# Performance work log

Measured on AMD Instinct MI355X. Metric: run time of the kernel, lower is better.

The kernel has to match this reference:

```python
import jax, jax.numpy as jnp
import numpy as np

P = 16           # patch size
E = P * P        # embed dim of MHA (must equal dim)
NH = 4           # num heads
HD = E // NH     # head dim


def setup_inputs() -> dict:
    key = jax.random.key(0)
    k1, k2, k3, k4, k5 = jax.random.split(key, 5)
    B, C, H, W = 2, 256, 256, 256
    scale = 1.0 / np.sqrt(E)
    return {
        "x": jax.random.normal(k1, (B, C, H, W), dtype=jnp.float32),
        "w_in": jax.random.normal(k2, (3 * E, E), dtype=jnp.float32) * scale,
        "b_in": jnp.zeros((3 * E,), dtype=jnp.float32),
        "w_out": jax.random.normal(k3, (E, E), dtype=jnp.float32) * scale,
        "b_out": jnp.zeros((E,), dtype=jnp.float32),
    }


def reference(x, w_in, b_in, w_out, b_out):
    B, C, H, W = x.shape
    nP = (H // P) * (W // P)
    # x.unfold(2,p,p).unfold(3,p,p).reshape(B,C,-1,p*p)
    patches = (
        x.reshape(B, C, H // P, P, W // P, P)
        .transpose(0, 1, 2, 4, 3, 5)
        .reshape(B, C, nP, E)
    )
    # permute(0,2,1,3).reshape(B*nP, C, p*p): batch=B*nP, seq=C, embed=E
    t = patches.transpose(0, 2, 1, 3).reshape(B * nP, C, E)

    qkv = t @ w_in.T + b_in                      # (N, C, 3E)
    q, k, v = jnp.split(qkv, 3, axis=-1)

    def to_heads(a):  # (N, C, E) -> (N, NH, C, HD)
        return a.reshape(B * nP, C, NH, HD).transpose(0, 2, 1, 3)

    q, k, v = to_heads(q), to_heads(k), to_heads(v)
    scores = jnp.einsum("nhqd,nhkd->nhqk", q * (HD ** -0.5), k)
    attn = jax.nn.softmax(scores, axis=-1)
    o = jnp.einsum("nhqk,nhkd->nhqd", attn, v)   # (N, NH, C, HD)
    o = o.transpose(0, 2, 1, 3).reshape(B * nP, C, E)
    o = o @ w_out.T + b_out
    # reshape(B, -1, C, p*p).permute(0, 2, 1, 3)
    return o.reshape(B, nP, C, E).transpose(0, 2, 1, 3)
```

## Files before the change

kernel.cpp:

```cpp
#include <hip/hip_runtime.h>
#include <hip/hip_bf16.h>

typedef __attribute__((ext_vector_type(8))) short s16x8;
typedef __attribute__((ext_vector_type(4))) float f32x4;

#define WS_SEG 67108864ULL

#if defined(__has_attribute)
#if __has_attribute(amdgpu_num_vgpr)
#define VGPR_CAP_128 __attribute__((amdgpu_num_vgpr(128)))
#else
#define VGPR_CAP_128
#endif
#else
#define VGPR_CAP_128
#endif

static __device__ __forceinline__ unsigned short f2bf(float f) {
    return __builtin_bit_cast(unsigned short, __float2bfloat16(f));
}
static __device__ __forceinline__ unsigned int pack2(float a, float b) {
    return (unsigned int)f2bf(a) | ((unsigned int)f2bf(b) << 16);
}
static __device__ __forceinline__ s16x8 u4cast(uint4 u) {
    return __builtin_bit_cast(s16x8, u);
}
static __device__ __forceinline__ void gl_lds16(const void* g, void* l) {
    __builtin_amdgcn_global_load_lds(
        (const __attribute__((address_space(1))) unsigned int*)g,
        (__attribute__((address_space(3))) unsigned int*)l, 16, 0, 0);
}

__global__ __launch_bounds__(256) void convw_frag(const float* __restrict__ wi,
                                                  unsigned short* __restrict__ wp) {
    int o8 = blockIdx.x * 256 + threadIdx.x;
    int nkc = o8 >> 10;
    int rem = o8 & 1023;
    int row = rem >> 2;
    int lk8 = (rem & 3) * 8;
    int Ni = nkc >> 3, kk = (nkc >> 1) & 3, kc = nkc & 1;
    const float* src = wi + ((size_t)(Ni * 256 + row)) * 256 + kk * 64 + kc * 32 + lk8;
    float4 a = *reinterpret_cast<const float4*>(src);
    float4 b = *reinterpret_cast<const float4*>(src + 4);
    uint4 o = { pack2(a.x, a.y), pack2(a.z, a.w), pack2(b.x, b.y), pack2(b.z, b.w) };
    *reinterpret_cast<uint4*>(wp + o8 * 8) = o;
}

__global__ __launch_bounds__(256) void convw_swz(const float* __restrict__ wi,
                                                 unsigned short* __restrict__ wb) {
    int i = (blockIdx.x * 256 + threadIdx.x) * 4;
    float4 v = *reinterpret_cast<const float4*>(wi + i);
    int bb = i * 2;
    int row = i >> 8;
    int dst = (bb & ~127) | ((bb & 127) ^ ((row & 7) << 4));
    uint2 o = { pack2(v.x, v.y), pack2(v.z, v.w) };
    *reinterpret_cast<uint2*>((char*)wb + dst) = o;
}

__global__ __launch_bounds__(256) void gather_swz(const float* __restrict__ x,
                                                  unsigned short* __restrict__ t) {
    int q = (blockIdx.x * 256 + threadIdx.x) * 4;
    int e = q & 255, c = (q >> 8) & 255, n = q >> 16;
    int b = n >> 8, p = n & 255;
    int xi = ((b * 256 + c) * 256 + (p >> 4) * 16 + (e >> 4)) * 256 + (p & 15) * 16 + (e & 15);
    float4 v = *reinterpret_cast<const float4*>(x + xi);
    int bb = q * 2;
    int row = q >> 8;
    int dst = (bb & ~127) | ((bb & 127) ^ ((row & 7) << 4));
    uint2 o = { pack2(v.x, v.y), pack2(v.z, v.w) };
    *reinterpret_cast<uint2*>((char*)t + dst) = o;
}

__global__ __launch_bounds__(256) void qkv11(
    const unsigned short* __restrict__ Ab,
    const unsigned short* __restrict__ Wp,
    const float* __restrict__ bias,
    unsigned short* __restrict__ Qo, unsigned short* __restrict__ Ko,
    unsigned short* __restrict__ Vt)
{
    __shared__ __align__(16) char AsB[65536];

    const int t = threadIdx.x, w = t >> 6, lane = t & 63;
    const int lr = lane & 15, lk = lane >> 4;
    const int wm = w >> 1, wn = w & 1;

    const int bm = blockIdx.x;
    const int n = bm >> 1;

    const char* Ag = (const char*)Ab + (size_t)bm * 65536;

    #pragma unroll
    for (int i = 0; i < 16; ++i) {
        int u = i * 256 + t;
        gl_lds16(Ag + u * 16, AsB + (i * 256 + w * 64) * 16);
    }
    __syncthreads();

    #pragma unroll 1
    for (int bn = 0; bn < 4; ++bn) {
        const int X = bn >> 1;
        const int half = bn & 1;
        f32x4 acc[4][4] = {};
        #pragma unroll
        for (int kk = 0; kk < 4; ++kk) {
            #pragma unroll
            for (int kc = 0; kc < 2; ++kc) {
                const char* wb = (const char*)Wp + (((X * 4 + kk) * 2 + kc) << 14);
                s16x8 bfr[4];
                #pragma unroll
                for (int fn = 0; fn < 4; ++fn)
                    bfr[fn] = *reinterpret_cast<const s16x8*>(
                        wb + ((half * 128 + wn * 64 + fn * 16 + lr) * 32 + lk * 8) * 2);
                s16x8 af[4];
                #pragma unroll
                for (int fm = 0; fm < 4; ++fm) {
                    int m = wm * 64 + fm * 16 + lr;
                    af[fm] = *reinterpret_cast<const s16x8*>(
                        AsB + m * 512 + kk * 128 + ((kc * 64 + lk * 16) ^ ((m & 7) << 4)));
                }
                __builtin_amdgcn_s_setprio(1);
                #pragma unroll
                for (int fm = 0; fm < 4; ++fm)
                    #pragma unroll
                    for (int fn = 0; fn < 4; ++fn)
                        acc[fm][fn] = __builtin_amdgcn_mfma_f32_16x16x32_bf16(bfr[fn], af[fm], acc[fm][fn], 0, 0, 0);
                __builtin_amdgcn_s_setprio(0);
            }
        }
        unsigned short* base = X ? Ko : Qo;
        const float qs = X ? 1.0f : 0.18033688011112042f;
        #pragma unroll
        for (int fn = 0; fn < 4; ++fn) {
            int col_local = wn * 64 + fn * 16 + lk * 4;
            int mc = half * 128 + col_local;
            f32x4 bv4 = *reinterpret_cast<const f32x4*>(bias + X * 256 + mc);
            int h = mc >> 6, d0 = mc & 63;
            #pragma unroll
            for (int fm = 0; fm < 4; ++fm) {
                int c = (bm & 1) * 128 + wm * 64 + fm * 16 + lr;
                uint2 st = { pack2((acc[fm][fn][0] + bv4[0]) * qs, (acc[fm][fn][1] + bv4[1]) * qs),
                             pack2((acc[fm][fn][2] + bv4[2]) * qs, (acc[fm][fn][3] + bv4[3]) * qs) };
                *reinterpret_cast<uint2*>(
                    (char*)base + (size_t)((n * 4 + h) * 256 + c) * 128 + d0 * 2) = st;
            }
        }
    }

    #pragma unroll 1
    for (int half = 0; half < 2; ++half) {
        f32x4 acc[4][4] = {};
        #pragma unroll
        for (int kk = 0; kk < 4; ++kk) {
            #pragma unroll
            for (int kc = 0; kc < 2; ++kc) {
                const char* wb = (const char*)Wp + (((2 * 4 + kk) * 2 + kc) << 14);
                s16x8 bfr[4];
                #pragma unroll
                for (int fn = 0; fn < 4; ++fn)
                    bfr[fn] = *reinterpret_cast<const s16x8*>(
                        wb + ((half * 128 + wn * 64 + fn * 16 + lr) * 32 + lk * 8) * 2);
                s16x8 af[4];
                #pragma unroll
                for (int fm = 0; fm < 4; ++fm) {
                    int m = wm * 64 + fm * 16 + lr;
                    af[fm] = *reinterpret_cast<const s16x8*>(
                        AsB + m * 512 + kk * 128 + ((kc * 64 + lk * 16) ^ ((m & 7) << 4)));
                }
                __builtin_amdgcn_s_setprio(1);
                #pragma unroll
                for (int fm = 0; fm < 4; ++fm)
                    #pragma unroll
                    for (int fn = 0; fn < 4; ++fn)
                        acc[fm][fn] = __builtin_amdgcn_mfma_f32_16x16x32_bf16(af[fm], bfr[fn], acc[fm][fn], 0, 0, 0);
                __builtin_amdgcn_s_setprio(0);
            }
        }
        #pragma unroll
        for (int fn = 0; fn < 4; ++fn) {
            int dcol_local = wn * 64 + fn * 16 + lr;
            int mc = half * 128 + dcol_local;
            float bv = bias[512 + mc];
            int h = mc >> 6, d = mc & 63;
            #pragma unroll
            for (int fm = 0; fm < 4; ++fm) {
                int c = (bm & 1) * 128 + wm * 64 + fm * 16 + lk * 4;
                uint2 st = { pack2(acc[fm][fn][0] + bv, acc[fm][fn][1] + bv),
                             pack2(acc[fm][fn][2] + bv, acc[fm][fn][3] + bv) };
                *reinterpret_cast<uint2*>(
                    (char*)Vt + (size_t)((n * 4 + h) * 64 + d) * 512 + c * 2) = st;
            }
        }
    }
}

__global__ __launch_bounds__(256) void gemm_out(
    const unsigned short* __restrict__ Ab,
    const unsigned short* __restrict__ Wb,
    const float* __restrict__ bias,
    float* __restrict__ Out)
{
    __shared__ __align__(16) char smem[32768];
    char* AsB = smem;
    char* BsB = smem + 16384;

    const int t = threadIdx.x, w = t >> 6, lane = t & 63;
    const int lr = lane & 15, lk = lane >> 4;
    const int wm = w >> 1, wn = w & 1;

    const int flat = blockIdx.x;
    const int xcd = flat & 7, idx = flat >> 3;
    const int bm = xcd * 128 + idx / 2;
    const int bn = idx % 2;

    const char* Ag = (const char*)Ab + (size_t)bm * 65536;
    const char* Bg = (const char*)Wb + (size_t)bn * 65536;

    f32x4 acc[4][4] = {};

    for (int kk = 0; kk < 4; ++kk) {
        #pragma unroll
        for (int i = 0; i < 4; ++i) {
            int u = (i * 4 + w) * 64 + lane;
            int row = u >> 3, cb = (u & 7) * 16;
            gl_lds16(Ag + row * 512 + kk * 128 + cb, AsB + (i * 4 + w) * 1024);
            gl_lds16(Bg + row * 512 + kk * 128 + cb, BsB + (i * 4 + w) * 1024);
        }
        __syncthreads();
        #pragma unroll
        for (int kc = 0; kc < 2; ++kc) {
            s16x8 af[4], bf[4];
            #pragma unroll
            for (int fm = 0; fm < 4; ++fm) {
                int r = wm * 64 + fm * 16 + lr;
                af[fm] = *reinterpret_cast<const s16x8*>(
                    AsB + r * 128 + ((kc * 64 + lk * 16) ^ ((r & 7) << 4)));
            }
            #pragma unroll
            for (int fn = 0; fn < 4; ++fn) {
                int cc = wn * 64 + fn * 16 + lr;
                bf[fn] = *reinterpret_cast<const s16x8*>(
                    BsB + cc * 128 + ((kc * 64 + lk * 16) ^ ((cc & 7) << 4)));
            }
            #pragma unroll
            for (int fm = 0; fm < 4; ++fm)
                #pragma unroll
                for (int fn = 0; fn < 4; ++fn)
                    acc[fm][fn] = __builtin_amdgcn_mfma_f32_16x16x32_bf16(bf[fn], af[fm], acc[fm][fn], 0, 0, 0);
        }
        if (kk < 3) __syncthreads();
    }

    #pragma unroll
    for (int fn = 0; fn < 4; ++fn) {
        int colg = bn * 128 + wn * 64 + fn * 16 + lk * 4;
        f32x4 bv4 = *reinterpret_cast<const f32x4*>(bias + colg);
        #pragma unroll
        for (int fm = 0; fm < 4; ++fm) {
            int rg = bm * 128 + wm * 64 + fm * 16 + lr;
            int nn = rg >> 8, c = rg & 255;
            int b = nn >> 8, p = nn & 255;
            f32x4 st = acc[fm][fn] + bv4;
            *reinterpret_cast<f32x4*>(
                Out + (((size_t)(b * 256 + c) * 256 + p) << 8) + colg) = st;
        }
    }
}

__global__ __launch_bounds__(1024) VGPR_CAP_128 void attn8(
    const unsigned short* __restrict__ Q,
    const unsigned short* __restrict__ K,
    const unsigned short* __restrict__ V,
    unsigned short* __restrict__ O)
{
    __shared__ __align__(16) char KsB[32768];
    __shared__ __align__(16) char VsB[32768];

    const int nh = blockIdx.x;
    const int n = nh >> 2, h = nh & 3;
    const int t = threadIdx.x, w = t >> 6, lane = t & 63;
    const int lr = lane & 15, lk = lane >> 4;

    const unsigned short* Qg = Q + (size_t)nh * 16384;
    const char* Kg = (const char*)K + (size_t)nh * 32768;
    const char* Vg = (const char*)V + (size_t)nh * 32768;

    #pragma unroll
    for (int i = 0; i < 2; ++i) {
        int u = i * 1024 + t;
        int row = u >> 3, cb = (u & 7) * 16;
        uint4 val = *reinterpret_cast<const uint4*>(Kg + u * 16);
        *reinterpret_cast<uint4*>(KsB + row * 128 + (cb ^ ((row & 7) << 4))) = val;
    }
    #pragma unroll
    for (int i = 0; i < 2; ++i) {
        int u = i * 1024 + t;
        int row = u >> 5, cb = (u & 31) * 16;
        uint4 val = *reinterpret_cast<const uint4*>(Vg + u * 16);
        *reinterpret_cast<uint4*>(VsB + row * 512 + (cb ^ ((row & 7) << 4))) = val;
    }
    __syncthreads();

    const int swz = (lr & 7) << 4;
    const int qt = w;

    s16x8 bq0 = *reinterpret_cast<const s16x8*>(Qg + (qt * 16 + lr) * 64 + lk * 8);
    s16x8 bq1 = *reinterpret_cast<const s16x8*>(Qg + (qt * 16 + lr) * 64 + 32 + lk * 8);

    f32x4 oacc[4] = {};
    float l = 0.f;

    #pragma unroll
    for (int kb = 0; kb < 8; ++kb) {
        const int rb0 = ((2 * kb) * 16 + lr) * 128;
        const int rb1 = ((2 * kb + 1) * 16 + lr) * 128;
        s16x8 a00 = *reinterpret_cast<const s16x8*>(KsB + rb0 + ((lk * 16) ^ swz));
        s16x8 a01 = *reinterpret_cast<const s16x8*>(KsB + rb0 + ((64 + lk * 16) ^ swz));
        s16x8 a10 = *reinterpret_cast<const s16x8*>(KsB + rb1 + ((lk * 16) ^ swz));
        s16x8 a11 = *reinterpret_cast<const s16x8*>(KsB + rb1 + ((64 + lk * 16) ^ swz));
        f32x4 s0 = { 0.f, 0.f, 0.f, 0.f }, s1 = { 0.f, 0.f, 0.f, 0.f };
        __builtin_amdgcn_s_setprio(1);
        s0 = __builtin_amdgcn_mfma_f32_16x16x32_bf16(a00, bq0, s0, 0, 0, 0);
        s0 = __builtin_amdgcn_mfma_f32_16x16x32_bf16(a01, bq1, s0, 0, 0, 0);
        s1 = __builtin_amdgcn_mfma_f32_16x16x32_bf16(a10, bq0, s1, 0, 0, 0);
        s1 = __builtin_amdgcn_mfma_f32_16x16x32_bf16(a11, bq1, s1, 0, 0, 0);
        __builtin_amdgcn_s_setprio(0);

        float p0 = exp2f(s0[0]), p1 = exp2f(s0[1]);
        float p2 = exp2f(s0[2]), p3 = exp2f(s0[3]);
        float p4 = exp2f(s1[0]), p5 = exp2f(s1[1]);
        float p6 = exp2f(s1[2]), p7 = exp2f(s1[3]);
        l += ((p0 + p1) + (p2 + p3)) + ((p4 + p5) + (p6 + p7));
        uint4 pk = { pack2(p0, p1), pack2(p2, p3), pack2(p4, p5), pack2(p6, p7) };
        s16x8 pf = u4cast(pk);

        __builtin_amdgcn_s_setprio(1);
        #pragma unroll
        for (int dt = 0; dt < 4; ++dt) {
            const char* vb = VsB + (dt * 16 + lr) * 512;
            uint2 v0 = *reinterpret_cast<const uint2*>(vb + ((kb * 64 + lk * 8) ^ swz));
            uint2 v1 = *reinterpret_cast<const uint2*>(vb + ((kb * 64 + lk * 8 + 32) ^ swz));
            uint4 uu = { v0.x, v0.y, v1.x, v1.y };
            oacc[dt] = __builtin_amdgcn_mfma_f32_16x16x32_bf16(u4cast(uu), pf, oacc[dt], 0, 0, 0);
        }
        __builtin_amdgcn_s_setprio(0);
    }

    l += __shfl_xor(l, 16);
    l += __shfl_xor(l, 32);
    const float rl = 1.0f / l;

    char* orow = (char*)O + (size_t)(n * 256 + qt * 16 + lr) * 512 + h * 128;
    #pragma unroll
    for (int dt = 0; dt < 4; ++dt) {
        uint2 st = { pack2(oacc[dt][0] * rl, oacc[dt][1] * rl),
                     pack2(oacc[dt][2] * rl, oacc[dt][3] * rl) };
        *reinterpret_cast<uint2*>(orow + ((dt * 32 + lk * 8) ^ swz)) = st;
    }
}

extern "C" void kernel_launch(void* const* d_in, const int* in_sizes, int n_in,
                              void* d_out, int out_size, void* d_ws, size_t ws_size,
                              hipStream_t stream) {
    const float* x     = (const float*)d_in[0];
    const float* w_in  = (const float*)d_in[1];
    const float* b_in  = (const float*)d_in[2];
    const float* w_out = (const float*)d_in[3];
    const float* b_out = (const float*)d_in[4];

    char* ws = (char*)d_ws;
    unsigned short* tO = (unsigned short*)(ws);
    unsigned short* Qw = (unsigned short*)(ws + WS_SEG);
    unsigned short* Kw = (unsigned short*)(ws + 2 * WS_SEG);
    unsigned short* Vw = (unsigned short*)(ws + 3 * WS_SEG);

    unsigned short* WbIn = (unsigned short*)((float*)d_out + out_size - 98304);

    convw_frag<<<96, 256, 0, stream>>>(w_in, WbIn);
    gather_swz<<<32768, 256, 0, stream>>>(x, tO);

    qkv11<<<1024, 256, 0, stream>>>(tO, WbIn, b_in, Qw, Kw, Vw);

    attn8<<<2048, 1024, 0, stream>>>(Qw, Kw, Vw, tO);

    unsigned short* WbOut = Kw;
    convw_swz<<<64, 256, 0, stream>>>(w_out, WbOut);

    gemm_out<<<2048, 256, 0, stream>>>(tO, WbOut, b_out, (float*)d_out);
}
```

Before: 321.7 us.

## Split QKV GEMM into per-N-tile blocks reading fragment-packed A directly from global

The gather kernel now writes the token matrix in MFMA fragment-packed order (per 128-row tile, per 32-wide k chunk), so the QKV kernel can load A fragments straight from global memory without staging through 64KB of LDS. The QKV GEMM is split from 1024 blocks that each loop over six output tiles into 6144 blocks that each compute one tile. Blocks are remapped so that the six blocks sharing an A tile land on the same XCD, to get L2 reuse. This cuts LDS use and raises occupancy and parallelism, at the cost of reading A six times from cache/global instead of once into LDS.

```diff
diff --git a/kernel.cpp b/kernel.cpp
--- a/kernel.cpp
+++ b/kernel.cpp
@@ -57,84 +57,82 @@
     *reinterpret_cast<uint2*>((char*)wb + dst) = o;
 }
 
-__global__ __launch_bounds__(256) void gather_swz(const float* __restrict__ x,
-                                                  unsigned short* __restrict__ t) {
+__global__ __launch_bounds__(256) void gather_frag(const float* __restrict__ x,
+                                                   unsigned short* __restrict__ tp) {
     int q = (blockIdx.x * 256 + threadIdx.x) * 4;
     int e = q & 255, c = (q >> 8) & 255, n = q >> 16;
     int b = n >> 8, p = n & 255;
     int xi = ((b * 256 + c) * 256 + (p >> 4) * 16 + (e >> 4)) * 256 + (p & 15) * 16 + (e & 15);
     float4 v = *reinterpret_cast<const float4*>(x + xi);
-    int bb = q * 2;
-    int row = q >> 8;
-    int dst = (bb & ~127) | ((bb & 127) ^ ((row & 7) << 4));
+    int mrow = n * 256 + c;
+    int mt = mrow >> 7, m = mrow & 127;
+    int kk = e >> 6, kc = (e >> 5) & 1, ke = e & 31;
+    size_t dst = ((size_t)(mt * 8 + kk * 2 + kc) << 13) + (size_t)(m * 32 + ke) * 2;
     uint2 o = { pack2(v.x, v.y), pack2(v.z, v.w) };
-    *reinterpret_cast<uint2*>((char*)t + dst) = o;
-}
-
-__global__ __launch_bounds__(256) void qkv11(
-    const unsigned short* __restrict__ Ab,
+    *reinterpret_cast<uint2*>((char*)tp + dst) = o;
+}
+
+__global__ __launch_bounds__(256) void qkv12(
+    const unsigned short* __restrict__ Tp,
     const unsigned short* __restrict__ Wp,
     const float* __restrict__ bias,
     unsigned short* __restrict__ Qo, unsigned short* __restrict__ Ko,
     unsigned short* __restrict__ Vt)
 {
-    __shared__ __align__(16) char AsB[65536];
-
     const int t = threadIdx.x, w = t >> 6, lane = t & 63;
     const int lr = lane & 15, lk = lane >> 4;
     const int wm = w >> 1, wn = w & 1;
 
-    const int bm = blockIdx.x;
-    const int n = bm >> 1;
-
-    const char* Ag = (const char*)Ab + (size_t)bm * 65536;
-
-    #pragma unroll
-    for (int i = 0; i < 16; ++i) {
-        int u = i * 256 + t;
-        gl_lds16(Ag + u * 16, AsB + (i * 256 + w * 64) * 16);
-    }
-    __syncthreads();
-
-    #pragma unroll 1
-    for (int bn = 0; bn < 4; ++bn) {
-        const int X = bn >> 1;
-        const int half = bn & 1;
-        f32x4 acc[4][4] = {};
-        #pragma unroll
-        for (int kk = 0; kk < 4; ++kk) {
-            #pragma unroll
-            for (int kc = 0; kc < 2; ++kc) {
-                const char* wb = (const char*)Wp + (((X * 4 + kk) * 2 + kc) << 14);
-                s16x8 bfr[4];
-                #pragma unroll
-                for (int fn = 0; fn < 4; ++fn)
-                    bfr[fn] = *reinterpret_cast<const s16x8*>(
-                        wb + ((half * 128 + wn * 64 + fn * 16 + lr) * 32 + lk * 8) * 2);
-                s16x8 af[4];
-                #pragma unroll
-                for (int fm = 0; fm < 4; ++fm) {
-                    int m = wm * 64 + fm * 16 + lr;
-                    af[fm] = *reinterpret_cast<const s16x8*>(
-                        AsB + m * 512 + kk * 128 + ((kc * 64 + lk * 16) ^ ((m & 7) << 4)));
-                }
-                __builtin_amdgcn_s_setprio(1);
+    const int flat = blockIdx.x;
+    const int xcd = flat & 7, idx = flat >> 3;
+    const int bm = xcd * 128 + idx / 6;
+    const int bn = idx % 6;
+    const int X = bn >> 1, half = bn & 1;
+
+    f32x4 acc[4][4] = {};
+
+    #pragma unroll
+    for (int kk = 0; kk < 4; ++kk) {
+        #pragma unroll
+        for (int kc = 0; kc < 2; ++kc) {
+            const char* tb = (const char*)Tp + ((size_t)(bm * 8 + kk * 2 + kc) << 13);
+            const char* wb = (const char*)Wp + (((X * 4 + kk) * 2 + kc) << 14);
+            s16x8 afr[4], bfr[4];
+            #pragma unroll
+            for (int fm = 0; fm < 4; ++fm)
+                afr[fm] = *reinterpret_cast<const s16x8*>(
+                    tb + ((wm * 64 + fm * 16 + lr) * 32 + lk * 8) * 2);
+            #pragma unroll
+            for (int fn = 0; fn < 4; ++fn)
+                bfr[fn] = *reinterpret_cast<const s16x8*>(
+                    wb + ((half * 128 + wn * 64 + fn * 16 + lr) * 32 + lk * 8) * 2);
+            if (X < 2) {
                 #pragma unroll
                 for (int fm = 0; fm < 4; ++fm)
                     #pragma unroll
                     for (int fn = 0; fn < 4; ++fn)
-                        acc[fm][fn] = __builtin_amdgcn_mfma_f32_16x16x32_bf16(bfr[fn], af[fm], acc[fm][fn], 0, 0, 0);
-                __builtin_amdgcn_s_setprio(0);
-            }
-        }
+                        acc[fm][fn] = __builtin_amdgcn_mfma_f32_16x16x32_bf16(bfr[fn], afr[fm], acc[fm][fn], 0, 0, 0);
+            } else {
+                #pragma unroll
+                for (int fm = 0; fm < 4; ++fm)
+                    #pragma unroll
+                    for (int fn = 0; fn < 4; ++fn)
+                        acc[fm][fn] = __builtin_amdgcn_mfma_f32_16x16x32_bf16(afr[fm], bfr[fn], acc[fm][fn], 0, 0, 0);
+            }
+        }
+    }
+
+    const int n = bm >> 1;
+
+    if (X < 2) {
         unsigned short* base = X ? Ko : Qo;
+        const int h0 = half * 2;
         const float qs = X ? 1.0f : 0.18033688011112042f;
         #pragma unroll
         for (int fn = 0; fn < 4; ++fn) {
             int col_local = wn * 64 + fn * 16 + lk * 4;
-            int mc = half * 128 + col_local;
-            f32x4 bv4 = *reinterpret_cast<const f32x4*>(bias + X * 256 + mc);
-            int h = mc >> 6, d0 = mc & 63;
+            f32x4 bv4 = *reinterpret_cast<const f32x4*>(bias + bn * 128 + col_local);
+            int h = h0 + (col_local >> 6), d0 = col_local & 63;
             #pragma unroll
             for (int fm = 0; fm < 4; ++fm) {
                 int c = (bm & 1) * 128 + wm * 64 + fm * 16 + lr;
@@ -144,50 +142,20 @@
                     (char*)base + (size_t)((n * 4 + h) * 256 + c) * 128 + d0 * 2) = st;
             }
         }
-    }
-
-    #pragma unroll 1
-    for (int half = 0; half < 2; ++half) {
-        f32x4 acc[4][4] = {};
-        #pragma unroll
-        for (int kk = 0; kk < 4; ++kk) {
-            #pragma unroll
-            for (int kc = 0; kc < 2; ++kc) {
-                const char* wb = (const char*)Wp + (((2 * 4 + kk) * 2 + kc) << 14);
-                s16x8 bfr[4];
-                #pragma unroll
-                for (int fn = 0; fn < 4; ++fn)
-                    bfr[fn] = *reinterpret_cast<const s16x8*>(
-                        wb + ((half * 128 + wn * 64 + fn * 16 + lr) * 32 + lk * 8) * 2);
-                s16x8 af[4];
-                #pragma unroll
-                for (int fm = 0; fm < 4; ++fm) {
-                    int m = wm * 64 + fm * 16 + lr;
-                    af[fm] = *reinterpret_cast<const s16x8*>(
-                        AsB + m * 512 + kk * 128 + ((kc * 64 + lk * 16) ^ ((m & 7) << 4)));
-                }
-                __builtin_amdgcn_s_setprio(1);
-                #pragma unroll
-                for (int fm = 0; fm < 4; ++fm)
-                    #pragma unroll
-                    for (int fn = 0; fn < 4; ++fn)
-                        acc[fm][fn] = __builtin_amdgcn_mfma_f32_16x16x32_bf16(af[fm], bfr[fn], acc[fm][fn], 0, 0, 0);
-                __builtin_amdgcn_s_setprio(0);
-            }
-        }
+    } else {
+        const int h0 = half * 2;
         #pragma unroll
         for (int fn = 0; fn < 4; ++fn) {
-            int dcol_local = wn * 64 + fn * 16 + lr;
-            int mc = half * 128 + dcol_local;
-            float bv = bias[512 + mc];
-            int h = mc >> 6, d = mc & 63;
+            int col_local = wn * 64 + fn * 16 + lr;
+            float bv = bias[bn * 128 + col_local];
+            int hl = col_local >> 6, d = col_local & 63;
             #pragma unroll
             for (int fm = 0; fm < 4; ++fm) {
                 int c = (bm & 1) * 128 + wm * 64 + fm * 16 + lk * 4;
                 uint2 st = { pack2(acc[fm][fn][0] + bv, acc[fm][fn][1] + bv),
                              pack2(acc[fm][fn][2] + bv, acc[fm][fn][3] + bv) };
                 *reinterpret_cast<uint2*>(
-                    (char*)Vt + (size_t)((n * 4 + h) * 64 + d) * 512 + c * 2) = st;
+                    (char*)Vt + (size_t)((n * 4 + h0 + hl) * 64 + d) * 512 + c * 2) = st;
             }
         }
     }
@@ -376,9 +344,9 @@
     unsigned short* WbIn = (unsigned short*)((float*)d_out + out_size - 98304);
 
     convw_frag<<<96, 256, 0, stream>>>(w_in, WbIn);
-    gather_swz<<<32768, 256, 0, stream>>>(x, tO);
-
-    qkv11<<<1024, 256, 0, stream>>>(tO, WbIn, b_in, Qw, Kw, Vw);
+    gather_frag<<<32768, 256, 0, stream>>>(x, tO);
+
+    qkv12<<<6144, 256, 0, stream>>>(tO, WbIn, b_in, Qw, Kw, Vw);
 
     attn8<<<2048, 1024, 0, stream>>>(Qw, Kw, Vw, tO);
 
```

Result: slower. 330.8 us (+2.8%).
